# Kernel optimization log

Measured on AMD Instinct MI355X. Metric: run time of the kernel, lower is better.

Reference implementation:

```python
import jax, jax.numpy as jnp
import numpy as np

EPS = 1e-6
SCALE = 1.0
GRID_HEIGHT = 4.0
GRID_RES_Y = 1.0


def _perspective(mat, vec):
    # mat [3,4], vec [...,3] -> (points [...,2], flag [...,3])
    homog = jnp.einsum('ij,...j->...i', mat[:, :3], vec) + mat[:, 3]
    pos = homog[..., 2:3] > 0
    flag = jnp.concatenate([pos, pos, jnp.ones_like(pos)], axis=-1).astype(homog.dtype)
    homog = homog * flag  # zero x,y behind camera; z kept (flag[...,-1]=True)
    return homog[..., :2] / homog[..., 2:3], flag


def _fisheye(pts, k, D, flag):
    cx, cy, fx, fy = k[0, 2], k[1, 2], k[0, 0], k[1, 1]
    x = (pts[..., 0] - cx) / fx
    y = (pts[..., 1] - cy) / fy
    r = jnp.sqrt(x * x + y * y)
    th = jnp.arctan(r)
    t2 = th * th
    rad = th * (1 + D[0] * t2 + D[1] * t2 ** 2 + D[2] * t2 ** 3 + D[5] * t2 ** 4) / r
    xd = x * rad * fx + cx
    yd = y * rad * fy + cy
    return jnp.stack([xd, yd], axis=-1) * flag[..., :2]


def _pinhole(pts, k, D, flag):
    cx, cy, fx, fy = k[0, 2], k[1, 2], k[0, 0], k[1, 1]
    x = (pts[..., 0] - cx) / fx
    y = (pts[..., 1] - cy) / fy
    k1, k2, k3, p1, p2 = D[0], D[1], D[2], D[3], D[4]
    r2 = x * x + y * y
    poly = 1 + k1 * r2 + k2 * r2 * r2 + k3 * r2 * r2 * r2
    xd = x * poly + (2 * p1 * x * y + p2 * (r2 + 2 * x * x))
    yd = y * poly + (p1 * (r2 + 2 * y * y) + 2 * p2 * x * y)
    return jnp.stack([xd * fx + cx, yd * fy + cy], axis=-1) * flag[..., :2]


def _bilinear(img, coords):
    # torch F.grid_sample(align_corners=True, padding_mode='border'); img [C,H,W], coords [...,2] in [-1,1]
    C, H, W = img.shape
    x = jnp.clip((coords[..., 0] + 1) * 0.5 * (W - 1), 0.0, W - 1)
    y = jnp.clip((coords[..., 1] + 1) * 0.5 * (H - 1), 0.0, H - 1)
    x0 = jnp.floor(x)
    y0 = jnp.floor(y)
    wx = x - x0
    wy = y - y0
    x0i = x0.astype(jnp.int32)
    y0i = y0.astype(jnp.int32)
    x1i = jnp.minimum(x0i + 1, W - 1)
    y1i = jnp.minimum(y0i + 1, H - 1)
    flat = img.reshape(C, H * W)

    def g(yi, xi):
        return jnp.take(flat, (yi * W + xi).reshape(-1), axis=1).reshape((C,) + coords.shape[:-1])

    v00 = g(y0i, x0i)
    v01 = g(y0i, x1i)
    v10 = g(y1i, x0i)
    v11 = g(y1i, x1i)
    return v00 * (1 - wx) * (1 - wy) + v01 * wx * (1 - wy) + v10 * (1 - wx) * wy + v11 * wx * wy


def _per_image(feature, k, imu2c, post_rot, post_tran, undist, corner):
    C, Hf, Wf = feature.shape
    calib = k @ imu2c                                  # [3,4]
    pts, flag = _perspective(calib, corner)            # pts [Ny,Zd,Xd,2]
    pts = jnp.where(undist[-1] == 1,
                    _fisheye(pts, k, undist, flag),
                    _pinhole(pts, k, undist, flag))
    pts = jnp.einsum('ij,...j->...i', post_rot[:2, :2], pts) + post_tran[:2]
    nc = jnp.clip(2.0 * (pts / SCALE) - 1.0, -1.0, 1.0)  # [Ny,Zd,Xd,2]
    s0, s1 = slice(None, -1), slice(1, None)
    # 8 voxel corners -> [8, Ny-1, D, Wd, 2]
    corners8 = jnp.stack([nc[a, b, c] for a in (s0, s1) for b in (s0, s1) for c in (s0, s1)], axis=0)
    left = corners8[..., 0].min(0)
    right = corners8[..., 0].max(0)
    top = corners8[..., 1].min(0)
    bot = corners8[..., 1].max(0)
    Nh, D, Wd = left.shape
    bbox = jnp.stack([left, top, right, bot], axis=-1).reshape(Nh, D * Wd, 4)
    area = (bbox[..., 2] - bbox[..., 0]) * (bbox[..., 3] - bbox[..., 1]) * Hf * Wf * 0.25 + EPS  # [Nh,P]
    integ = jnp.cumsum(jnp.cumsum(feature, axis=-1), axis=-2)  # integral image [C,Hf,Wf]
    tl = _bilinear(integ, bbox[..., 0:2])
    br = _bilinear(integ, bbox[..., 2:4])
    tr = _bilinear(integ, jnp.stack([bbox[..., 2], bbox[..., 1]], axis=-1))
    bl = _bilinear(integ, jnp.stack([bbox[..., 0], bbox[..., 3]], axis=-1))
    vox = (tl + br - tr - bl) / area * (area > EPS)    # [C,Nh,P]
    return vox.reshape(C * Nh, D, Wd)                  # neck == '2d'


def _forward(features, ks, imu2cs, post_rots, post_trans, undists, grid):
    ys = -jnp.arange(0.0, GRID_HEIGHT, GRID_RES_Y) + GRID_HEIGHT / 2.0
    y_corners = jnp.stack([jnp.zeros_like(ys), ys, jnp.zeros_like(ys)], axis=-1)  # [Ny,3]
    corners = grid[:, None] + y_corners[None, :, None, None, :]                   # [B,Ny,Zd,Xd,3]
    per_cam = jax.vmap(_per_image, in_axes=(0, 0, 0, 0, 0, 0, None))

    def per_batch(f, k, m, pr, pt, ud, c):
        # drop_idx = [] -> all cameras kept; max over cameras
        return per_cam(f, k, m, pr, pt, ud, c).max(axis=0)

    return jax.vmap(per_batch)(features, ks, imu2cs, post_rots, post_trans, undists, corners)


def setup_inputs():
    key = jax.random.key(0)
    B, N, C, Hf, Wf = 1, 6, 64, 64, 176
    Zd = Xd = 129
    kf, ku = jax.random.split(key, 2)
    features = jax.random.normal(kf, (B, N, C, Hf, Wf), jnp.float32)
    # intrinsics (realistic pinhole values keep the projection numerically sane)
    K = np.zeros((B, N, 3, 3), np.float32)
    K[..., 0, 0] = 600.0
    K[..., 1, 1] = 600.0
    K[..., 0, 2] = 704.0
    K[..., 1, 2] = 256.0
    K[..., 2, 2] = 1.0
    ks = jnp.asarray(K)
    # extrinsics: per-camera yaw + small translation
    m = np.zeros((B, N, 3, 4), np.float32)
    for i in range(N):
        th = 0.25 * (i - 2.5)
        R = np.array([[np.cos(th), 0.0, np.sin(th)],
                      [0.0, 1.0, 0.0],
                      [-np.sin(th), 0.0, np.cos(th)]], np.float32)
        m[:, i, :, :3] = R
        m[:, i, :, 3] = np.array([0.1 * i, -1.5, 0.2], np.float32)
    imu2cs = jnp.asarray(m)
    pr = np.zeros((B, N, 3, 3), np.float32)
    pr[..., 0, 0] = 1.0 / 1408.0
    pr[..., 1, 1] = 1.0 / 512.0
    pr[..., 2, 2] = 1.0
    post_rots = jnp.asarray(pr)
    post_trans = jnp.zeros((B, N, 3), jnp.float32)
    und = 0.01 * np.array(jax.random.normal(ku, (B, N, 7)), np.float32)
    und[..., 6] = 0.0
    und[:, :3, 6] = 1.0  # first 3 cameras fisheye, rest pinhole
    undists = jnp.asarray(und)
    x = np.linspace(-40.0, 40.0, Xd, dtype=np.float32)
    z = np.linspace(3.0, 80.0, Zd, dtype=np.float32)
    zz, xx = np.meshgrid(z, x, indexing='ij')
    g = np.stack([xx, np.zeros_like(xx), zz], axis=-1)[None]  # [1,Zd,Xd,3]
    grid = jnp.asarray(np.broadcast_to(g, (B, Zd, Xd, 3)).copy())
    return {"features": features, "ks": ks, "imu2cs": imu2cs, "post_rots": post_rots,
            "post_trans": post_trans, "undists": undists, "grid": grid}


def reference(features, ks, imu2cs, post_rots, post_trans, undists, grid):
    return _forward(features, ks, imu2cs, post_rots, post_trans, undists, grid)
```

## Files before the change

### kernel.cpp

```cpp
#include <hip/hip_runtime.h>
#include <math.h>

#define NCAM 6
#define C_CH 64
#define HF   64
#define WF   176
#define GDIM 129
#define NY   4
#define NH   3
#define DD   128
#define WDIM 128
#define NP   (DD*WDIM)

struct alignas(64) BoxP {
    int   r0, r1, r2, r3;
    int   c0, c1, c2, c3;
    float wxL, wxR, wyT, wyB;
    float area;
    int   pad0, pad1, pad2;
};
static_assert(sizeof(BoxP) == 64, "BoxP size");

__device__ __forceinline__ int rfl_i(int x) {
    return __builtin_amdgcn_readfirstlane(x);
}
__device__ __forceinline__ float rfl_f(float x) {
    return __builtin_bit_cast(float, __builtin_amdgcn_readfirstlane(__builtin_bit_cast(int, x)));
}

__global__ void k_project(const float* __restrict__ ks,
                          const float* __restrict__ imu2cs,
                          const float* __restrict__ post_rots,
                          const float* __restrict__ post_trans,
                          const float* __restrict__ undists,
                          const float* __restrict__ grid,
                          float2* __restrict__ ncbuf)
{
    const int n   = blockIdx.y;
    const int idx = blockIdx.x * blockDim.x + threadIdx.x;
    const int per = NY * GDIM * GDIM;
    if (idx >= per) return;
    const int ny  = idx / (GDIM * GDIM);
    const int rem = idx % (GDIM * GDIM);
    const int gz  = rem / GDIM;
    const int gx  = rem % GDIM;

    const float* k  = ks         + n * 9;
    const float* m  = imu2cs     + n * 12;
    const float* pr = post_rots  + n * 9;
    const float* pt = post_trans + n * 3;
    const float* D  = undists    + n * 7;

    float cal[12];
    #pragma unroll
    for (int i = 0; i < 3; ++i)
        #pragma unroll
        for (int j = 0; j < 4; ++j)
            cal[i*4+j] = k[i*3+0]*m[0*4+j] + k[i*3+1]*m[1*4+j] + k[i*3+2]*m[2*4+j];

    const float vx = grid[(gz*GDIM + gx)*3 + 0];
    const float vy = 2.0f - (float)ny;
    const float vz = grid[(gz*GDIM + gx)*3 + 2];

    const float hx = cal[0]*vx + cal[1]*vy + cal[2]*vz  + cal[3];
    const float hy = cal[4]*vx + cal[5]*vy + cal[6]*vz  + cal[7];
    const float hz = cal[8]*vx + cal[9]*vy + cal[10]*vz + cal[11];

    const float fl = (hz > 0.0f) ? 1.0f : 0.0f;
    const float px = (hx * fl) / hz;
    const float py = (hy * fl) / hz;

    const float fx = k[0], fy = k[4], cx = k[2], cy = k[5];
    const float x = (px - cx) / fx;
    const float y = (py - cy) / fy;

    float xd, yd;
    if (D[6] == 1.0f) {
        const float r  = sqrtf(x*x + y*y);
        const float th = atanf(r);
        const float t2 = th * th;
        const float t4 = t2 * t2;
        const float rad = th * (1.0f + D[0]*t2 + D[1]*t4 + D[2]*(t2*t4) + D[5]*(t4*t4)) / r;
        xd = x * rad * fx + cx;
        yd = y * rad * fy + cy;
    } else {
        const float k1 = D[0], k2 = D[1], k3 = D[2], p1 = D[3], p2 = D[4];
        const float r2 = x*x + y*y;
        const float poly = 1.0f + k1*r2 + k2*r2*r2 + k3*r2*r2*r2;
        const float xdd = x*poly + (2.0f*p1*x*y + p2*(r2 + 2.0f*x*x));
        const float ydd = y*poly + (p1*(r2 + 2.0f*y*y) + 2.0f*p2*x*y);
        xd = xdd * fx + cx;
        yd = ydd * fy + cy;
    }
    xd *= fl; yd *= fl;

    const float qx = pr[0]*xd + pr[1]*yd + pt[0];
    const float qy = pr[3]*xd + pr[4]*yd + pt[1];
    const float ncx = fminf(fmaxf(2.0f*qx - 1.0f, -1.0f), 1.0f);
    const float ncy = fminf(fmaxf(2.0f*qy - 1.0f, -1.0f), 1.0f);
    ncbuf[((n*NY + ny)*GDIM + gz)*GDIM + gx] = make_float2(ncx, ncy);
}

__global__ __launch_bounds__(256) void k_rowcum(const float* __restrict__ feat,
                                                float* __restrict__ integ)
{
    __shared__ float T[WF * 65];
    __shared__ float S[4][C_CH];
    __shared__ float OFF[4][C_CH];
    const int h   = blockIdx.x;
    const int n   = blockIdx.y;
    const int tid = threadIdx.x;

    for (int idx = tid; idx < C_CH * WF; idx += 256) {
        const int cc = idx / WF;
        const int w  = idx % WF;
        T[w*65 + cc] = feat[((size_t)(n*C_CH + cc)*HF + h)*WF + w];
    }
    __syncthreads();
    {
        const int cc = tid & 63, seg = tid >> 6;
        const int w0 = seg * 44;
        float run = 0.0f;
        #pragma unroll
        for (int i = 0; i < 44; ++i) {
            run += T[(w0 + i)*65 + cc];
            T[(w0 + i)*65 + cc] = run;
        }
        S[seg][cc] = run;
    }
    __syncthreads();
    {
        const int cc = tid & 63, seg = tid >> 6;
        float off = 0.0f;
        #pragma unroll
        for (int s = 0; s < 3; ++s)
            if (s < seg) off += S[s][cc];
        OFF[seg][cc] = off;
    }
    __syncthreads();
    float* outp = integ + (size_t)(n*HF + h) * (WF * C_CH);
    for (int idx = tid; idx < WF * C_CH; idx += 256) {
        const int w  = idx >> 6;
        const int cc = idx & 63;
        outp[idx] = T[w*65 + cc] + OFF[w/44][cc];
    }
}

__global__ void k_colcum(float* __restrict__ integ)
{
    const int t = blockIdx.x * blockDim.x + threadIdx.x;
    const int n = blockIdx.y;
    if (t >= WF * C_CH) return;
    float* p = integ + (size_t)n * HF * WF * C_CH + t;
    float run = 0.0f;
    #pragma unroll
    for (int h = 0; h < HF; ++h) {
        run += p[(size_t)h * (WF * C_CH)];
        p[(size_t)h * (WF * C_CH)] = run;
    }
}

__global__ void k_boxparams(const float2* __restrict__ ncbuf, BoxP* __restrict__ bp)
{
    const int idx = blockIdx.x * blockDim.x + threadIdx.x;
    if (idx >= NCAM * NH * NP) return;
    const int n  = idx / (NH * NP);
    const int r  = idx % (NH * NP);
    const int nh = r / NP;
    const int p  = r % NP;
    const int d  = p / WDIM;
    const int wd = p % WDIM;

    float left = 1e30f, right = -1e30f, top = 1e30f, bot = -1e30f;
    #pragma unroll
    for (int a = 0; a < 2; ++a)
        #pragma unroll
        for (int b = 0; b < 2; ++b)
            #pragma unroll
            for (int cc = 0; cc < 2; ++cc) {
                const float2 v = ncbuf[((n*NY + nh + a)*GDIM + d + b)*GDIM + wd + cc];
                left  = fminf(left,  v.x);  right = fmaxf(right, v.x);
                top   = fminf(top,   v.y);  bot   = fmaxf(bot,   v.y);
            }

    const float area = (right - left) * (bot - top) * (float)HF * (float)WF * 0.25f + 1e-6f;

    const float xLp = fminf(fmaxf((left  + 1.0f) * 0.5f * (float)(WF-1), 0.0f), (float)(WF-1));
    const float xRp = fminf(fmaxf((right + 1.0f) * 0.5f * (float)(WF-1), 0.0f), (float)(WF-1));
    const float yTp = fminf(fmaxf((top   + 1.0f) * 0.5f * (float)(HF-1), 0.0f), (float)(HF-1));
    const float yBp = fminf(fmaxf((bot   + 1.0f) * 0.5f * (float)(HF-1), 0.0f), (float)(HF-1));
    const float xL0 = floorf(xLp), xR0 = floorf(xRp), yT0 = floorf(yTp), yB0 = floorf(yBp);

    const int ixL0 = (int)xL0, ixR0 = (int)xR0, iyT0 = (int)yT0, iyB0 = (int)yB0;
    const int ixL1 = min(ixL0 + 1, WF-1), ixR1 = min(ixR0 + 1, WF-1);
    const int iyT1 = min(iyT0 + 1, HF-1), iyB1 = min(iyB0 + 1, HF-1);

    BoxP o;
    o.r0 = iyT0 * (WF*C_CH*4); o.r1 = iyT1 * (WF*C_CH*4);
    o.r2 = iyB0 * (WF*C_CH*4); o.r3 = iyB1 * (WF*C_CH*4);
    o.c0 = ixL0 * (C_CH*4);    o.c1 = ixL1 * (C_CH*4);
    o.c2 = ixR0 * (C_CH*4);    o.c3 = ixR1 * (C_CH*4);
    o.wxL = xLp - xL0; o.wxR = xRp - xR0; o.wyT = yTp - yT0; o.wyB = yBp - yB0;
    o.area = area; o.pad0 = 0; o.pad1 = 0; o.pad2 = 0;
    bp[idx] = o;
}

__global__ __launch_bounds__(256) void k_sample(const float* __restrict__ integ,
                                                const BoxP* __restrict__ bp,
                                                float* __restrict__ out)
{
    __shared__ float sm[C_CH][17];
    const int nh   = blockIdx.y;
    const int p0   = blockIdx.x * 16;
    const int tid  = threadIdx.x;
    const int wave = __builtin_amdgcn_readfirstlane(tid >> 6);
    const int c    = tid & 63;

    #pragma unroll 1
    for (int j = 0; j < 4; ++j) {
        const int pj = p0 + wave*4 + j;
        float vmax = -3.402823466e38f;
        #pragma unroll 1
        for (int n = 0; n < NCAM; ++n) {
            const BoxP* bpp = &bp[(n*NH + nh)*NP + pj];
            const float area = rfl_f(bpp->area);
            if (!(area > 1e-6f)) {
                vmax = fmaxf(vmax, 0.0f);
                continue;
            }
            const int r0 = rfl_i(bpp->r0), r1 = rfl_i(bpp->r1);
            const int r2 = rfl_i(bpp->r2), r3 = rfl_i(bpp->r3);
            const int c0 = rfl_i(bpp->c0), c1 = rfl_i(bpp->c1);
            const int c2 = rfl_i(bpp->c2), c3 = rfl_i(bpp->c3);
            const float wxL = rfl_f(bpp->wxL), wxR = rfl_f(bpp->wxR);
            const float wyT = rfl_f(bpp->wyT), wyB = rfl_f(bpp->wyB);

            const char* base = (const char*)integ + (size_t)n * (HF*WF*C_CH*4);
            auto LD = [&](int ro, int co) -> float {
                return ((const float*)(base + (size_t)(ro + co)))[c];
            };
            const float t0L0 = LD(r0,c0), t0L1 = LD(r0,c1), t0R0 = LD(r0,c2), t0R1 = LD(r0,c3);
            const float t1L0 = LD(r1,c0), t1L1 = LD(r1,c1), t1R0 = LD(r1,c2), t1R1 = LD(r1,c3);
            const float b0L0 = LD(r2,c0), b0L1 = LD(r2,c1), b0R0 = LD(r2,c2), b0R1 = LD(r2,c3);
            const float b1L0 = LD(r3,c0), b1L1 = LD(r3,c1), b1R0 = LD(r3,c2), b1R1 = LD(r3,c3);

            const float A0 = fmaf(wxL, t0L1 - t0L0, t0L0);
            const float B0 = fmaf(wxR, t0R1 - t0R0, t0R0);
            const float A1 = fmaf(wxL, t1L1 - t1L0, t1L0);
            const float B1 = fmaf(wxR, t1R1 - t1R0, t1R0);
            const float A2 = fmaf(wxL, b0L1 - b0L0, b0L0);
            const float B2 = fmaf(wxR, b0R1 - b0R0, b0R0);
            const float A3 = fmaf(wxL, b1L1 - b1L0, b1L0);
            const float B3 = fmaf(wxR, b1R1 - b1R0, b1R0);
            const float d0 = A0 - B0, d1 = A1 - B1;
            const float e0 = B2 - A2, e1 = B3 - A3;
            const float s = fmaf(wyT, d1 - d0, d0) + fmaf(wyB, e1 - e0, e0);
            const float val = s * __builtin_amdgcn_rcpf(area);
            vmax = fmaxf(vmax, val);
        }
        sm[c][wave*4 + j] = vmax;
    }
    __syncthreads();
    for (int idx = tid; idx < C_CH * 16; idx += 256) {
        const int cc = idx >> 4;
        const int jj = idx & 15;
        out[(size_t)(cc*NH + nh)*NP + p0 + jj] = sm[cc][jj];
    }
}

extern "C" void kernel_launch(void* const* d_in, const int* in_sizes, int n_in,
                              void* d_out, int out_size, void* d_ws, size_t ws_size,
                              hipStream_t stream)
{
    const float* feats      = (const float*)d_in[0];
    const float* ks         = (const float*)d_in[1];
    const float* imu2cs     = (const float*)d_in[2];
    const float* post_rots  = (const float*)d_in[3];
    const float* post_trans = (const float*)d_in[4];
    const float* undists    = (const float*)d_in[5];
    const float* grid       = (const float*)d_in[6];
    float* out = (float*)d_out;

    char* ws = (char*)d_ws;
    size_t off = 0;
    float2* ncbuf = (float2*)(ws + off);
    off += sizeof(float2) * NCAM * NY * GDIM * GDIM;
    off = (off + 255) & ~(size_t)255;
    float* integ = (float*)(ws + off);
    off += sizeof(float) * NCAM * HF * WF * C_CH;
    off = (off + 255) & ~(size_t)255;
    BoxP* bp = (BoxP*)(ws + off);
    off += sizeof(BoxP) * NCAM * NH * NP;
    (void)ws_size; (void)in_sizes; (void)n_in; (void)out_size;

    dim3 g1((NY*GDIM*GDIM + 255)/256, NCAM);
    k_project<<<g1, 256, 0, stream>>>(ks, imu2cs, post_rots, post_trans, undists, grid, ncbuf);

    dim3 g2a(HF, NCAM);
    k_rowcum<<<g2a, 256, 0, stream>>>(feats, integ);

    dim3 g2b((WF*C_CH + 255)/256, NCAM);
    k_colcum<<<g2b, 256, 0, stream>>>(integ);

    dim3 g3((NCAM*NH*NP + 255)/256);
    k_boxparams<<<g3, 256, 0, stream>>>(ncbuf, bp);

    dim3 g4(NP/16, NH);
    k_sample<<<g4, 256, 0, stream>>>(integ, bp, out);
}
```

Before: 161.0 us.

## Pack 2x2 integral-image neighbours into float4 quads for vectorized box sampling

The column-cumulative pass becomes k_quadcol, which writes each integral-image texel together with its right, lower and lower-right neighbours as one float4. The sampler then issues four 16-byte loads per box instead of sixteen scalar loads, and BoxP shrinks to four precomputed corner offsets. The sampler block also covers 32 points instead of 16. The cost is a quadcol buffer four times the size of the integral image, written redundantly, plus an extra shared-memory scan pass.

```diff
diff --git a/kernel.cpp b/kernel.cpp
--- a/kernel.cpp
+++ b/kernel.cpp
@@ -12,14 +12,13 @@
 #define WDIM 128
 #define NP   (DD*WDIM)
 
-struct alignas(64) BoxP {
-    int   r0, r1, r2, r3;
-    int   c0, c1, c2, c3;
+struct alignas(16) BoxP {
+    int   oTL, oTR, oBL, oBR;
     float wxL, wxR, wyT, wyB;
     float area;
     int   pad0, pad1, pad2;
 };
-static_assert(sizeof(BoxP) == 64, "BoxP size");
+static_assert(sizeof(BoxP) == 48, "BoxP size");
 
 __device__ __forceinline__ int rfl_i(int x) {
     return __builtin_amdgcn_readfirstlane(x);
@@ -102,7 +101,7 @@
 }
 
 __global__ __launch_bounds__(256) void k_rowcum(const float* __restrict__ feat,
-                                                float* __restrict__ integ)
+                                                float* __restrict__ rowsum)
 {
     __shared__ float T[WF * 65];
     __shared__ float S[4][C_CH];
@@ -138,7 +137,7 @@
         OFF[seg][cc] = off;
     }
     __syncthreads();
-    float* outp = integ + (size_t)(n*HF + h) * (WF * C_CH);
+    float* outp = rowsum + (size_t)(n*HF + h) * (WF * C_CH);
     for (int idx = tid; idx < WF * C_CH; idx += 256) {
         const int w  = idx >> 6;
         const int cc = idx & 63;
@@ -146,17 +145,54 @@
     }
 }
 
-__global__ void k_colcum(float* __restrict__ integ)
-{
-    const int t = blockIdx.x * blockDim.x + threadIdx.x;
-    const int n = blockIdx.y;
-    if (t >= WF * C_CH) return;
-    float* p = integ + (size_t)n * HF * WF * C_CH + t;
-    float run = 0.0f;
+__global__ __launch_bounds__(256) void k_quadcol(const float* __restrict__ rowsum,
+                                                 float4* __restrict__ qbuf)
+{
+    __shared__ float A[HF][C_CH];
+    __shared__ float Bb[HF][C_CH];
+    __shared__ float tA[4][C_CH], tB[4][C_CH];
+    const int x  = blockIdx.x;
+    const int n  = blockIdx.y;
+    const int x1 = min(x + 1, WF - 1);
+    const int c  = threadIdx.x & 63;
+    const int hq = threadIdx.x >> 6;
+
+    const float* base0 = rowsum + (size_t)n*HF*WF*C_CH + (size_t)x  * C_CH + c;
+    const float* base1 = rowsum + (size_t)n*HF*WF*C_CH + (size_t)x1 * C_CH + c;
+    float run0 = 0.0f, run1 = 0.0f;
     #pragma unroll
-    for (int h = 0; h < HF; ++h) {
-        run += p[(size_t)h * (WF * C_CH)];
-        p[(size_t)h * (WF * C_CH)] = run;
+    for (int i = 0; i < 16; ++i) {
+        const int h = hq*16 + i;
+        run0 += base0[(size_t)h * (WF*C_CH)];
+        run1 += base1[(size_t)h * (WF*C_CH)];
+        A[h][c]  = run0;
+        Bb[h][c] = run1;
+    }
+    tA[hq][c] = run0;
+    tB[hq][c] = run1;
+    __syncthreads();
+    {
+        float offA = 0.0f, offB = 0.0f;
+        #pragma unroll
+        for (int s = 0; s < 3; ++s)
+            if (s < hq) { offA += tA[s][c]; offB += tB[s][c]; }
+        #pragma unroll
+        for (int i = 0; i < 16; ++i) {
+            const int h = hq*16 + i;
+            A[h][c]  += offA;
+            Bb[h][c] += offB;
+        }
+    }
+    __syncthreads();
+    float4* qb = qbuf + ((size_t)n*HF*WF + x) * C_CH + c;
+    #pragma unroll
+    for (int i = 0; i < 16; ++i) {
+        const int h  = hq*16 + i;
+        const int hn = min(h + 1, HF - 1);
+        float4 q;
+        q.x = A[h][c];  q.y = Bb[h][c];
+        q.z = A[hn][c]; q.w = Bb[hn][c];
+        qb[(size_t)h * (WF*C_CH)] = q;
     }
 }
 
@@ -191,34 +227,32 @@
     const float yBp = fminf(fmaxf((bot   + 1.0f) * 0.5f * (float)(HF-1), 0.0f), (float)(HF-1));
     const float xL0 = floorf(xLp), xR0 = floorf(xRp), yT0 = floorf(yTp), yB0 = floorf(yBp);
 
-    const int ixL0 = (int)xL0, ixR0 = (int)xR0, iyT0 = (int)yT0, iyB0 = (int)yB0;
-    const int ixL1 = min(ixL0 + 1, WF-1), ixR1 = min(ixR0 + 1, WF-1);
-    const int iyT1 = min(iyT0 + 1, HF-1), iyB1 = min(iyB0 + 1, HF-1);
+    const int rT = (int)yT0 * (WF*C_CH*16);
+    const int rB = (int)yB0 * (WF*C_CH*16);
+    const int cL = (int)xL0 * (C_CH*16);
+    const int cR = (int)xR0 * (C_CH*16);
 
     BoxP o;
-    o.r0 = iyT0 * (WF*C_CH*4); o.r1 = iyT1 * (WF*C_CH*4);
-    o.r2 = iyB0 * (WF*C_CH*4); o.r3 = iyB1 * (WF*C_CH*4);
-    o.c0 = ixL0 * (C_CH*4);    o.c1 = ixL1 * (C_CH*4);
-    o.c2 = ixR0 * (C_CH*4);    o.c3 = ixR1 * (C_CH*4);
+    o.oTL = rT + cL; o.oTR = rT + cR; o.oBL = rB + cL; o.oBR = rB + cR;
     o.wxL = xLp - xL0; o.wxR = xRp - xR0; o.wyT = yTp - yT0; o.wyB = yBp - yB0;
     o.area = area; o.pad0 = 0; o.pad1 = 0; o.pad2 = 0;
     bp[idx] = o;
 }
 
-__global__ __launch_bounds__(256) void k_sample(const float* __restrict__ integ,
+__global__ __launch_bounds__(256) void k_sample(const float4* __restrict__ qbuf,
                                                 const BoxP* __restrict__ bp,
                                                 float* __restrict__ out)
 {
-    __shared__ float sm[C_CH][17];
+    __shared__ float sm[C_CH][33];
     const int nh   = blockIdx.y;
-    const int p0   = blockIdx.x * 16;
+    const int p0   = blockIdx.x * 32;
     const int tid  = threadIdx.x;
     const int wave = __builtin_amdgcn_readfirstlane(tid >> 6);
     const int c    = tid & 63;
 
     #pragma unroll 1
-    for (int j = 0; j < 4; ++j) {
-        const int pj = p0 + wave*4 + j;
+    for (int j = 0; j < 8; ++j) {
+        const int pj = p0 + wave*8 + j;
         float vmax = -3.402823466e38f;
         #pragma unroll 1
         for (int n = 0; n < NCAM; ++n) {
@@ -228,42 +262,38 @@
                 vmax = fmaxf(vmax, 0.0f);
                 continue;
             }
-            const int r0 = rfl_i(bpp->r0), r1 = rfl_i(bpp->r1);
-            const int r2 = rfl_i(bpp->r2), r3 = rfl_i(bpp->r3);
-            const int c0 = rfl_i(bpp->c0), c1 = rfl_i(bpp->c1);
-            const int c2 = rfl_i(bpp->c2), c3 = rfl_i(bpp->c3);
+            const int oTL = rfl_i(bpp->oTL), oTR = rfl_i(bpp->oTR);
+            const int oBL = rfl_i(bpp->oBL), oBR = rfl_i(bpp->oBR);
             const float wxL = rfl_f(bpp->wxL), wxR = rfl_f(bpp->wxR);
             const float wyT = rfl_f(bpp->wyT), wyB = rfl_f(bpp->wyB);
 
-            const char* base = (const char*)integ + (size_t)n * (HF*WF*C_CH*4);
-            auto LD = [&](int ro, int co) -> float {
-                return ((const float*)(base + (size_t)(ro + co)))[c];
+            const char* qb = (const char*)qbuf + (size_t)n * ((size_t)HF*WF*C_CH*16);
+            auto LDQ = [&](int off) -> float4 {
+                return ((const float4*)(qb + (size_t)off))[c];
             };
-            const float t0L0 = LD(r0,c0), t0L1 = LD(r0,c1), t0R0 = LD(r0,c2), t0R1 = LD(r0,c3);
-            const float t1L0 = LD(r1,c0), t1L1 = LD(r1,c1), t1R0 = LD(r1,c2), t1R1 = LD(r1,c3);
-            const float b0L0 = LD(r2,c0), b0L1 = LD(r2,c1), b0R0 = LD(r2,c2), b0R1 = LD(r2,c3);
-            const float b1L0 = LD(r3,c0), b1L1 = LD(r3,c1), b1R0 = LD(r3,c2), b1R1 = LD(r3,c3);
-
-            const float A0 = fmaf(wxL, t0L1 - t0L0, t0L0);
-            const float B0 = fmaf(wxR, t0R1 - t0R0, t0R0);
-            const float A1 = fmaf(wxL, t1L1 - t1L0, t1L0);
-            const float B1 = fmaf(wxR, t1R1 - t1R0, t1R0);
-            const float A2 = fmaf(wxL, b0L1 - b0L0, b0L0);
-            const float B2 = fmaf(wxR, b0R1 - b0R0, b0R0);
-            const float A3 = fmaf(wxL, b1L1 - b1L0, b1L0);
-            const float B3 = fmaf(wxR, b1R1 - b1R0, b1R0);
-            const float d0 = A0 - B0, d1 = A1 - B1;
-            const float e0 = B2 - A2, e1 = B3 - A3;
-            const float s = fmaf(wyT, d1 - d0, d0) + fmaf(wyB, e1 - e0, e0);
-            const float val = s * __builtin_amdgcn_rcpf(area);
-            vmax = fmaxf(vmax, val);
+            const float4 qTL = LDQ(oTL);
+            const float4 qTR = LDQ(oTR);
+            const float4 qBL = LDQ(oBL);
+            const float4 qBR = LDQ(oBR);
+
+            auto BIL = [&](const float4& q, float wx, float wy) -> float {
+                const float m0 = fmaf(wx, q.y - q.x, q.x);
+                const float m1 = fmaf(wx, q.w - q.z, q.z);
+                return fmaf(wy, m1 - m0, m0);
+            };
+            const float tl = BIL(qTL, wxL, wyT);
+            const float tr = BIL(qTR, wxR, wyT);
+            const float bl = BIL(qBL, wxL, wyB);
+            const float br = BIL(qBR, wxR, wyB);
+            const float s  = (tl + br) - (tr + bl);
+            vmax = fmaxf(vmax, s * __builtin_amdgcn_rcpf(area));
         }
-        sm[c][wave*4 + j] = vmax;
-    }
-    __syncthreads();
-    for (int idx = tid; idx < C_CH * 16; idx += 256) {
-        const int cc = idx >> 4;
-        const int jj = idx & 15;
+        sm[c][wave*8 + j] = vmax;
+    }
+    __syncthreads();
+    for (int idx = tid; idx < C_CH * 32; idx += 256) {
+        const int cc = idx >> 5;
+        const int jj = idx & 31;
         out[(size_t)(cc*NH + nh)*NP + p0 + jj] = sm[cc][jj];
     }
 }
@@ -286,8 +316,11 @@
     float2* ncbuf = (float2*)(ws + off);
     off += sizeof(float2) * NCAM * NY * GDIM * GDIM;
     off = (off + 255) & ~(size_t)255;
-    float* integ = (float*)(ws + off);
+    float* rowsum = (float*)(ws + off);
     off += sizeof(float) * NCAM * HF * WF * C_CH;
+    off = (off + 255) & ~(size_t)255;
+    float4* qbuf = (float4*)(ws + off);
+    off += sizeof(float4) * (size_t)NCAM * HF * WF * C_CH;
     off = (off + 255) & ~(size_t)255;
     BoxP* bp = (BoxP*)(ws + off);
     off += sizeof(BoxP) * NCAM * NH * NP;
@@ -297,14 +330,14 @@
     k_project<<<g1, 256, 0, stream>>>(ks, imu2cs, post_rots, post_trans, undists, grid, ncbuf);
 
     dim3 g2a(HF, NCAM);
-    k_rowcum<<<g2a, 256, 0, stream>>>(feats, integ);
-
-    dim3 g2b((WF*C_CH + 255)/256, NCAM);
-    k_colcum<<<g2b, 256, 0, stream>>>(integ);
+    k_rowcum<<<g2a, 256, 0, stream>>>(feats, rowsum);
+
+    dim3 g2b(WF, NCAM);
+    k_quadcol<<<g2b, 256, 0, stream>>>(rowsum, qbuf);
 
     dim3 g3((NCAM*NH*NP + 255)/256);
     k_boxparams<<<g3, 256, 0, stream>>>(ncbuf, bp);
 
-    dim3 g4(NP/16, NH);
-    k_sample<<<g4, 256, 0, stream>>>(integ, bp, out);
-}
+    dim3 g4(NP/32, NH);
+    k_sample<<<g4, 256, 0, stream>>>(qbuf, bp, out);
+}
```

New measurement: 158.0 us. Within noise of the previous version (-1.9%).
